# Kernel optimization log

Hardware: AMD Instinct MI355X
Metric: run time of the kernel (lower is better)

Reference implementation:

```python
import jax, jax.numpy as jnp
import numpy as np

NEG_INF = -10000000000.0
HEADS = 16


def setup_inputs() -> dict:
    key = jax.random.key(0)
    ks = jax.random.split(key, 12)
    B, S, E = 2, 2048, 1024
    sc = 1.0 / np.sqrt(E)
    inp = {
        "input_queries": jax.random.normal(ks[0], (B, S, E), jnp.float32),
        "input_keys": jax.random.normal(ks[1], (B, S, E), jnp.float32),
        "input_values": jax.random.normal(ks[2], (B, S, E), jnp.float32),
        # causal mask: True where attention is disallowed (masked_fill where mask==True)
        "mask": jnp.triu(jnp.ones((S, S), jnp.bool_), k=1)[None, None],
        "Wq": jax.random.normal(ks[3], (E, E), jnp.float32) * sc,
        "bq": jax.random.normal(ks[4], (E,), jnp.float32) * 0.01,
        "Wk": jax.random.normal(ks[5], (E, E), jnp.float32) * sc,
        "bk": jax.random.normal(ks[6], (E,), jnp.float32) * 0.01,
        "Wv": jax.random.normal(ks[7], (E, E), jnp.float32) * sc,
        "bv": jax.random.normal(ks[8], (E,), jnp.float32) * 0.01,
        "Wo": jax.random.normal(ks[9], (E, E), jnp.float32) * sc,
        "bo": jax.random.normal(ks[10], (E,), jnp.float32) * 0.01,
    }
    return inp


def reference(input_queries, input_keys, input_values, mask, Wq, bq, Wk, bk, Wv, bv, Wo, bo):
    B, S, E = input_queries.shape
    H = HEADS
    D = E // H
    # torch Linear: y = x @ W.T + b
    q = (input_queries @ Wq.T + bq).reshape(B, S, H, D).transpose(0, 2, 1, 3)  # bhsd
    k = (input_keys @ Wk.T + bk).reshape(B, S, H, D).transpose(0, 2, 1, 3)
    v = (input_values @ Wv.T + bv).reshape(B, S, H, D).transpose(0, 2, 1, 3)
    scores = jnp.einsum('bhqd,bhkd->bhqk', q, k) / jnp.sqrt(jnp.asarray(D, q.dtype))
    scores = jnp.where(mask, jnp.asarray(NEG_INF, scores.dtype), scores)
    attn = jax.nn.softmax(scores, axis=-1)
    out = jnp.einsum('bhqk,bhkd->bhqd', attn, v).transpose(0, 2, 1, 3).reshape(B, S, E)
    return out @ Wo.T + bo
```

## Files before the change

kernel.cpp:

```cpp
#include <hip/hip_runtime.h>
#include <hip/hip_bf16.h>

#define DEVI __device__ __forceinline__

using bf16x8 = __attribute__((ext_vector_type(8))) short;
using f32x4  = __attribute__((ext_vector_type(4))) float;
using f32x16 = __attribute__((ext_vector_type(16))) float;

#define LOG2E 1.4426950408889634f

DEVI unsigned short f2bf(float f){
  unsigned int u = __float_as_uint(f);
  return (unsigned short)((u + 0x7fffu + ((u>>16)&1u)) >> 16);
}

DEVI unsigned int cvt_pk_bf16(float lo, float hi){
  unsigned int r;
  asm("v_cvt_pk_bf16_f32 %0, %1, %2" : "=v"(r) : "v"(lo), "v"(hi));
  return r;
}

#if __has_builtin(__builtin_amdgcn_exp2f)
#define EXP2(x) __builtin_amdgcn_exp2f(x)
#else
#define EXP2(x) exp2f(x)
#endif

DEVI void gload_lds16(const unsigned short* src, unsigned short* lds){
  __builtin_amdgcn_global_load_lds((const __attribute__((address_space(1))) void*)src,
                                   (__attribute__((address_space(3))) void*)lds, 16, 0, 0);
}

DEVI bf16x8 mk8(unsigned w0, unsigned w1, unsigned w2, unsigned w3){
  union { unsigned u[4]; bf16x8 v; } x;
  x.u[0]=w0; x.u[1]=w1; x.u[2]=w2; x.u[3]=w3;
  return x.v;
}

__global__ __launch_bounds__(256) void convert_kernel(
  const float* __restrict__ Xq, const float* __restrict__ Xk, const float* __restrict__ Xv,
  const float* __restrict__ Wq, const float* __restrict__ Wk, const float* __restrict__ Wv,
  const float* __restrict__ Wo, unsigned short* __restrict__ ws)
{
  const int y = blockIdx.y;
  const float* src;
  unsigned short* dst;
  int n4;
  if (y < 3){
    src = (y==0)?Xq:((y==1)?Xk:Xv);
    dst = ws + (size_t)y*4194304;
    n4 = 1048576;
  } else {
    src = (y==3)?Wq:((y==4)?Wk:((y==5)?Wv:Wo));
    dst = ws + 12582912 + (size_t)(y-3)*1048576;
    n4 = 262144;
  }
  const int stride = gridDim.x * 256;
  for (int i = blockIdx.x*256 + threadIdx.x; i < n4; i += stride){
    float4 v = ((const float4*)src)[i];
    uint2 u;
    u.x = cvt_pk_bf16(v.x, v.y);
    u.y = cvt_pk_bf16(v.z, v.w);
    ((uint2*)dst)[i] = u;
  }
}

__global__ __launch_bounds__(256) void proj_qkv_kernel(
  const unsigned short* __restrict__ Xb, const unsigned short* __restrict__ Wb,
  const float* __restrict__ Bq, const float* __restrict__ Bk, const float* __restrict__ Bv,
  unsigned short* __restrict__ Qo, unsigned short* __restrict__ Ko, unsigned short* __restrict__ Vo)
{
  const int p = blockIdx.y;
  const unsigned short* __restrict__ A = Xb + (size_t)p*4194304;
  const unsigned short* __restrict__ B = Wb + (size_t)p*1048576;
  const float* __restrict__ Bb = (p==0)?Bq:((p==1)?Bk:Bv);
  unsigned short* __restrict__ Out = (p==0)?Qo:((p==1)?Ko:Vo);
  const float oscale = (p==0)?(0.125f*LOG2E):1.0f;

  const int tm = blockIdx.x >> 3, tn = blockIdx.x & 7;
  const int m0 = tm*128, n0 = tn*128;
  const int tid = threadIdx.x;
  const int w = tid>>6, l = tid&63;
  const int wr = w>>1, wc = w&1;
  const int lg = l>>4, lr = l&15;

  __shared__ unsigned short As[128*64];
  __shared__ unsigned short Bs[128*64];

  f32x4 acc[4][4];
  #pragma unroll
  for (int i=0;i<4;i++)
    #pragma unroll
    for (int j=0;j<4;j++){ f32x4 z = {0.f,0.f,0.f,0.f}; acc[i][j] = z; }

  for (int kt=0; kt<1024; kt+=64){
    #pragma unroll
    for (int i=0;i<4;i++){
      int rbase = w*32 + i*8;
      gload_lds16(A + (size_t)(m0 + rbase + (l>>3))*1024 + kt + (l&7)*8, As + rbase*64);
      gload_lds16(B + (size_t)(n0 + rbase + (l>>3))*1024 + kt + (l&7)*8, Bs + rbase*64);
    }
    __syncthreads();

    #pragma unroll
    for (int ck=0;ck<2;ck++){
      bf16x8 af[4], bfr[4];
      #pragma unroll
      for (int f=0;f<4;f++){
        af[f]  = *(const bf16x8*)(As + (wr*64 + f*16 + lr)*64 + ck*32 + lg*8);
        bfr[f] = *(const bf16x8*)(Bs + (wc*64 + f*16 + lr)*64 + ck*32 + lg*8);
      }
      #pragma unroll
      for (int fr=0;fr<4;fr++)
        #pragma unroll
        for (int fc=0;fc<4;fc++)
          acc[fr][fc] = __builtin_amdgcn_mfma_f32_16x16x32_bf16(af[fr], bfr[fc], acc[fr][fc], 0,0,0);
    }
    __syncthreads();
  }

  if (p == 2){
    #pragma unroll
    for (int fc=0;fc<4;fc++){
      int n = n0 + wc*64 + fc*16 + lr;
      float bias = Bb[n];
      int h = n>>6, d = n&63;
      #pragma unroll
      for (int fr=0;fr<4;fr++){
        int m = m0 + wr*64 + fr*16 + lg*4;
        int b = m>>11, s = m & 2047;
        uint2 u;
        u.x = cvt_pk_bf16(acc[fr][fc][0]+bias, acc[fr][fc][1]+bias);
        u.y = cvt_pk_bf16(acc[fr][fc][2]+bias, acc[fr][fc][3]+bias);
        *(uint2*)(Out + (((size_t)((b<<4)+h)*64 + d)*2048 + s)) = u;
      }
    }
  } else {
    #pragma unroll
    for (int fc=0;fc<4;fc++){
      int n = n0 + wc*64 + fc*16 + lr;
      float bias = Bb[n];
      int h = n>>6, d = n&63;
      #pragma unroll
      for (int fr=0;fr<4;fr++){
        #pragma unroll
        for (int r=0;r<4;r++){
          int m = m0 + wr*64 + fr*16 + lg*4 + r;
          int b = m>>11, s = m & 2047;
          float v = (acc[fr][fc][r] + bias) * oscale;
          Out[ ((size_t)((b<<4)+h)*2048 + (size_t)s)*64 + d ] = f2bf(v);
        }
      }
    }
  }
}

__global__ __launch_bounds__(256,2) void attn_kernel(
  const unsigned short* __restrict__ Q, const unsigned short* __restrict__ Kg,
  const unsigned short* __restrict__ Vt, unsigned short* __restrict__ AO)
{
  const int idx = blockIdx.x;
  const int qt = 15 - (idx >> 5);
  const int bh = idx & 31;
  const size_t base = (size_t)bh * 131072;
  const int q0 = qt * 128;
  const int tid = threadIdx.x, w = tid>>6, l = tid&63;
  const int lq = l & 31, hi = l >> 5;
  const int qq = q0 + w*32 + lq;

  __shared__ unsigned short Ks[2][4096];
  __shared__ unsigned short Vs[2][4096];

  bf16x8 qf[4];
  {
    const unsigned short* qp = Q + base + (size_t)qq*64;
    #pragma unroll
    for (int s=0;s<4;s++) qf[s] = *(const bf16x8*)(qp + s*16 + hi*8);
  }

  f32x16 oacc[2];
  #pragma unroll
  for (int dt=0;dt<2;dt++)
    #pragma unroll
    for (int r=0;r<16;r++) oacc[dt][r] = 0.f;
  float m_i = -INFINITY, l_i = 0.f;

  const int NT = 2*qt + 2;

  auto stage = [&](int kt, int half){
    const int kv0 = kt*64;
    #pragma unroll
    for (int i=0;i<2;i++){
      int c = tid + i*256;
      int row = c>>3;
      int kc = (c&7) ^ (row&7);
      gload_lds16(Kg + base + (size_t)(kv0+row)*64 + kc*8, &Ks[half][0] + c*8);
      gload_lds16(Vt + base + (size_t)row*2048 + kv0 + kc*8, &Vs[half][0] + c*8);
    }
  };

  stage(0, 0);
  __syncthreads();

  for (int kt=0; kt<NT; kt++){
    const int cur = kt & 1;
    if (kt+1 < NT) stage(kt+1, cur^1);
    const int kv0 = kt*64;

    f32x16 sacc[2];
    #pragma unroll
    for (int kvt=0;kvt<2;kvt++)
      #pragma unroll
      for (int r=0;r<16;r++) sacc[kvt][r] = 0.f;

    __builtin_amdgcn_s_setprio(1);
    #pragma unroll
    for (int kvt=0;kvt<2;kvt++){
      int row = kvt*32 + lq;
      const char* kb = (const char*)&Ks[cur][0] + row*128;
      int swz = (row&7)<<4;
      #pragma unroll
      for (int s=0;s<4;s++){
        bf16x8 kf = *(const bf16x8*)(kb + ((s*32 + hi*16) ^ swz));
        sacc[kvt] = __builtin_amdgcn_mfma_f32_32x32x16_bf16(kf, qf[s], sacc[kvt], 0,0,0);
      }
    }
    __builtin_amdgcn_s_setprio(0);

    #pragma unroll
    for (int kvt=0;kvt<2;kvt++){
      if (kv0 + kvt*32 + 31 > q0 + w*32){
        #pragma unroll
        for (int r=0;r<16;r++){
          int kvv = kv0 + kvt*32 + (r&3) + 8*(r>>2) + 4*hi;
          if (kvv > qq) sacc[kvt][r] = -1e30f;
        }
      }
    }

    float mt = sacc[0][0];
    #pragma unroll
    for (int kvt=0;kvt<2;kvt++)
      #pragma unroll
      for (int r=0;r<16;r++) mt = fmaxf(mt, sacc[kvt][r]);
    mt = fmaxf(mt, __shfl_xor(mt, 32));

    if (__any(mt > m_i + 8.f)){
      float mn = fmaxf(m_i, mt);
      float sc = EXP2(m_i - mn);
      m_i = mn;
      l_i *= sc;
      #pragma unroll
      for (int dt=0;dt<2;dt++)
        #pragma unroll
        for (int r=0;r<16;r++) oacc[dt][r] *= sc;
    }
    float rs = 0.f;
    #pragma unroll
    for (int kvt=0;kvt<2;kvt++)
      #pragma unroll
      for (int r=0;r<16;r++){
        float pv = EXP2(sacc[kvt][r] - m_i);
        sacc[kvt][r] = pv;
        rs += pv;
      }
    rs += __shfl_xor(rs, 32);
    l_i += rs;

    unsigned pa[8], pb[8], sa[8], sb[8];
    #pragma unroll
    for (int g=0; g<8; g++){
      int kvt = g>>2, gl = g&3;
      pa[g] = cvt_pk_bf16(sacc[kvt][4*gl+0], sacc[kvt][4*gl+1]);
      pb[g] = cvt_pk_bf16(sacc[kvt][4*gl+2], sacc[kvt][4*gl+3]);
      sa[g] = __shfl_xor(pa[g], 32);
      sb[g] = __shfl_xor(pb[g], 32);
    }
    bf16x8 pfrag[4];
    #pragma unroll
    for (int s=0;s<4;s++){
      int g0 = (s>>1)*4 + 2*(s&1);
      unsigned w0 = hi ? sa[g0+1] : pa[g0];
      unsigned w1 = hi ? sb[g0+1] : pb[g0];
      unsigned w2 = hi ? pa[g0+1] : sa[g0];
      unsigned w3 = hi ? pb[g0+1] : sb[g0];
      pfrag[s] = mk8(w0, w1, w2, w3);
    }

    __builtin_amdgcn_s_setprio(1);
    #pragma unroll
    for (int dt=0;dt<2;dt++){
      int row = dt*32 + lq;
      const char* vb = (const char*)&Vs[cur][0] + row*128;
      int swz = (row&7)<<4;
      #pragma unroll
      for (int s=0;s<4;s++){
        bf16x8 vf = *(const bf16x8*)(vb + ((s*32 + hi*16) ^ swz));
        oacc[dt] = __builtin_amdgcn_mfma_f32_32x32x16_bf16(vf, pfrag[s], oacc[dt], 0,0,0);
      }
    }
    __builtin_amdgcn_s_setprio(0);

    __syncthreads();
  }

  unsigned short* Es = &Ks[0][0] + w*2048;
  float inv = 1.0f / l_i;
  {
    char* eb = (char*)Es + lq*128;
    int swz = (lq&7)<<4;
    #pragma unroll
    for (int dt=0;dt<2;dt++)
      #pragma unroll
      for (int g=0;g<4;g++){
        int d0 = dt*32 + 8*g + 4*hi;
        unsigned u0 = cvt_pk_bf16(oacc[dt][4*g+0]*inv, oacc[dt][4*g+1]*inv);
        unsigned u1 = cvt_pk_bf16(oacc[dt][4*g+2]*inv, oacc[dt][4*g+3]*inv);
        *(unsigned*)(eb + ((d0*2    ) ^ swz)) = u0;
        *(unsigned*)(eb + ((d0*2 + 4) ^ swz)) = u1;
      }
  }
  const int b = bh>>4, h = bh&15;
  {
    const char* rb = (const char*)Es + lq*128;
    int swz = (lq&7)<<4;
    unsigned short* op = AO + ((size_t)b*2048 + (q0 + w*32 + lq))*1024 + h*64 + hi*32;
    #pragma unroll
    for (int j=0;j<2;j++){
      bf16x8 v = *(const bf16x8*)(rb + ((hi*64 + j*16) ^ swz));
      *(bf16x8*)(op + j*8) = v;
    }
    #pragma unroll
    for (int j=2;j<4;j++){
      bf16x8 v = *(const bf16x8*)(rb + ((hi*64 + j*16) ^ swz));
      *(bf16x8*)(op + j*8) = v;
    }
  }
}

__global__ __launch_bounds__(256) void proj_out_kernel(
  const unsigned short* __restrict__ A, const unsigned short* __restrict__ B,
  const float* __restrict__ Bb, float* __restrict__ Out)
{
  const int tm = blockIdx.x >> 3, tn = blockIdx.x & 7;
  const int m0 = tm*128, n0 = tn*128;
  const int tid = threadIdx.x;
  const int w = tid>>6, l = tid&63;
  const int wr = w>>1, wc = w&1;
  const int lg = l>>4, lr = l&15;

  __shared__ unsigned short As[128*64];
  __shared__ unsigned short Bs[128*64];

  f32x4 acc[4][4];
  #pragma unroll
  for (int i=0;i<4;i++)
    #pragma unroll
    for (int j=0;j<4;j++){ f32x4 z = {0.f,0.f,0.f,0.f}; acc[i][j] = z; }

  for (int kt=0; kt<1024; kt+=64){
    #pragma unroll
    for (int i=0;i<4;i++){
      int rbase = w*32 + i*8;
      gload_lds16(A + (size_t)(m0 + rbase + (l>>3))*1024 + kt + (l&7)*8, As + rbase*64);
      gload_lds16(B + (size_t)(n0 + rbase + (l>>3))*1024 + kt + (l&7)*8, Bs + rbase*64);
    }
    __syncthreads();

    #pragma unroll
    for (int ck=0;ck<2;ck++){
      bf16x8 af[4], bfr[4];
      #pragma unroll
      for (int f=0;f<4;f++){
        af[f]  = *(const bf16x8*)(As + (wr*64 + f*16 + lr)*64 + ck*32 + lg*8);
        bfr[f] = *(const bf16x8*)(Bs + (wc*64 + f*16 + lr)*64 + ck*32 + lg*8);
      }
      #pragma unroll
      for (int fr=0;fr<4;fr++)
        #pragma unroll
        for (int fc=0;fc<4;fc++)
          acc[fr][fc] = __builtin_amdgcn_mfma_f32_16x16x32_bf16(af[fr], bfr[fc], acc[fr][fc], 0,0,0);
    }
    __syncthreads();
  }

  #pragma unroll
  for (int fc=0;fc<4;fc++){
    int n = n0 + wc*64 + fc*16 + lr;
    float bias = Bb[n];
    #pragma unroll
    for (int fr=0;fr<4;fr++){
      #pragma unroll
      for (int r=0;r<4;r++){
        int m = m0 + wr*64 + fr*16 + lg*4 + r;
        Out[(size_t)m*1024 + n] = acc[fr][fc][r] + bias;
      }
    }
  }
}

extern "C" void kernel_launch(void* const* d_in, const int* in_sizes, int n_in,
                              void* d_out, int out_size, void* d_ws, size_t ws_size,
                              hipStream_t stream)
{
  const float* Xq = (const float*)d_in[0];
  const float* Xk = (const float*)d_in[1];
  const float* Xv = (const float*)d_in[2];
  const float* Wq = (const float*)d_in[4];
  const float* bq = (const float*)d_in[5];
  const float* Wk = (const float*)d_in[6];
  const float* bk = (const float*)d_in[7];
  const float* Wv = (const float*)d_in[8];
  const float* bv = (const float*)d_in[9];
  const float* Wo = (const float*)d_in[10];
  const float* bo = (const float*)d_in[11];

  unsigned short* ws  = (unsigned short*)d_ws;
  unsigned short* Xb  = ws;
  unsigned short* Wb  = ws + 12582912;
  unsigned short* Qw  = ws + 16777216;
  unsigned short* Kw  = ws + 20971520;
  unsigned short* Vw  = ws + 25165824;
  unsigned short* AOw = ws + 29360128;
  float* out = (float*)d_out;

  convert_kernel<<<dim3(512,7), 256, 0, stream>>>(Xq,Xk,Xv,Wq,Wk,Wv,Wo, ws);
  proj_qkv_kernel<<<dim3(256,3), 256, 0, stream>>>(Xb, Wb, bq,bk,bv, Qw,Kw,Vw);
  attn_kernel<<<512, 256, 0, stream>>>(Qw,Kw,Vw,AOw);
  proj_out_kernel<<<256, 256, 0, stream>>>(AOw, Wb + 3*1048576, bo, out);
}
```

Before: 254.7 us.

## Double-buffer GEMM LDS tiles, XOR-swizzle LDS layout, remap blocks per XCD

Both projection GEMMs now double-buffer the A/B tiles in LDS, so the global-to-LDS load of the next K-slice overlaps the MFMA work on the current one. LDS rows are XOR-swizzled by row index to avoid bank conflicts on the fragment reads. Block indices are remapped so each XCD gets contiguous M-tiles that share A rows, which should improve L2 reuse. The price is twice the LDS per block, which may lower occupancy.

Measured after the change: 249.2 us. -2.2%, faster.

```diff
diff --git a/kernel.cpp b/kernel.cpp
--- a/kernel.cpp
+++ b/kernel.cpp
@@ -70,22 +70,27 @@
   const float* __restrict__ Bq, const float* __restrict__ Bk, const float* __restrict__ Bv,
   unsigned short* __restrict__ Qo, unsigned short* __restrict__ Ko, unsigned short* __restrict__ Vo)
 {
-  const int p = blockIdx.y;
+  const int L = blockIdx.x;
+  const int xcd = L & 7, g = L >> 3;
+  const int combo = xcd*12 + (g>>3);
+  const int tn = g & 7;
+  const int p  = combo >> 5;
+  const int tm = combo & 31;
+
   const unsigned short* __restrict__ A = Xb + (size_t)p*4194304;
   const unsigned short* __restrict__ B = Wb + (size_t)p*1048576;
   const float* __restrict__ Bb = (p==0)?Bq:((p==1)?Bk:Bv);
   unsigned short* __restrict__ Out = (p==0)?Qo:((p==1)?Ko:Vo);
   const float oscale = (p==0)?(0.125f*LOG2E):1.0f;
 
-  const int tm = blockIdx.x >> 3, tn = blockIdx.x & 7;
   const int m0 = tm*128, n0 = tn*128;
   const int tid = threadIdx.x;
   const int w = tid>>6, l = tid&63;
   const int wr = w>>1, wc = w&1;
   const int lg = l>>4, lr = l&15;
 
-  __shared__ unsigned short As[128*64];
-  __shared__ unsigned short Bs[128*64];
+  __shared__ unsigned short As[2][8192];
+  __shared__ unsigned short Bs[2][8192];
 
   f32x4 acc[4][4];
   #pragma unroll
@@ -93,22 +98,34 @@
     #pragma unroll
     for (int j=0;j<4;j++){ f32x4 z = {0.f,0.f,0.f,0.f}; acc[i][j] = z; }
 
-  for (int kt=0; kt<1024; kt+=64){
+  const int sub = l>>3;
+  const int kc  = (l&7) ^ sub;
+  auto stage = [&](int kt, int h){
     #pragma unroll
     for (int i=0;i<4;i++){
       int rbase = w*32 + i*8;
-      gload_lds16(A + (size_t)(m0 + rbase + (l>>3))*1024 + kt + (l&7)*8, As + rbase*64);
-      gload_lds16(B + (size_t)(n0 + rbase + (l>>3))*1024 + kt + (l&7)*8, Bs + rbase*64);
-    }
-    __syncthreads();
+      gload_lds16(A + (size_t)(m0+rbase+sub)*1024 + kt + kc*8, &As[h][0] + rbase*64);
+      gload_lds16(B + (size_t)(n0+rbase+sub)*1024 + kt + kc*8, &Bs[h][0] + rbase*64);
+    }
+  };
+
+  stage(0, 0);
+  asm volatile("s_waitcnt vmcnt(0)" ::: "memory");
+  __builtin_amdgcn_s_barrier();
+
+  int cur = 0;
+  for (int kt6=0; kt6<16; kt6++){
+    if (kt6 < 15) stage((kt6+1)*64, cur^1);
 
     #pragma unroll
     for (int ck=0;ck<2;ck++){
       bf16x8 af[4], bfr[4];
       #pragma unroll
       for (int f=0;f<4;f++){
-        af[f]  = *(const bf16x8*)(As + (wr*64 + f*16 + lr)*64 + ck*32 + lg*8);
-        bfr[f] = *(const bf16x8*)(Bs + (wc*64 + f*16 + lr)*64 + ck*32 + lg*8);
+        int ra = wr*64 + f*16 + lr;
+        af[f]  = *(const bf16x8*)((const char*)&As[cur][0] + ra*128 + ((ck*64 + lg*16) ^ ((ra&7)<<4)));
+        int rb = wc*64 + f*16 + lr;
+        bfr[f] = *(const bf16x8*)((const char*)&Bs[cur][0] + rb*128 + ((ck*64 + lg*16) ^ ((rb&7)<<4)));
       }
       #pragma unroll
       for (int fr=0;fr<4;fr++)
@@ -116,7 +133,10 @@
         for (int fc=0;fc<4;fc++)
           acc[fr][fc] = __builtin_amdgcn_mfma_f32_16x16x32_bf16(af[fr], bfr[fc], acc[fr][fc], 0,0,0);
     }
-    __syncthreads();
+
+    asm volatile("s_waitcnt vmcnt(0)" ::: "memory");
+    __builtin_amdgcn_s_barrier();
+    cur ^= 1;
   }
 
   if (p == 2){
@@ -342,15 +362,18 @@
   const unsigned short* __restrict__ A, const unsigned short* __restrict__ B,
   const float* __restrict__ Bb, float* __restrict__ Out)
 {
-  const int tm = blockIdx.x >> 3, tn = blockIdx.x & 7;
+  const int L = blockIdx.x;
+  const int xcd = L & 7, g = L >> 3;
+  const int tm = xcd*4 + (g>>3);
+  const int tn = g & 7;
   const int m0 = tm*128, n0 = tn*128;
   const int tid = threadIdx.x;
   const int w = tid>>6, l = tid&63;
   const int wr = w>>1, wc = w&1;
   const int lg = l>>4, lr = l&15;
 
-  __shared__ unsigned short As[128*64];
-  __shared__ unsigned short Bs[128*64];
+  __shared__ unsigned short As[2][8192];
+  __shared__ unsigned short Bs[2][8192];
 
   f32x4 acc[4][4];
   #pragma unroll
@@ -358,22 +381,34 @@
     #pragma unroll
     for (int j=0;j<4;j++){ f32x4 z = {0.f,0.f,0.f,0.f}; acc[i][j] = z; }
 
-  for (int kt=0; kt<1024; kt+=64){
+  const int sub = l>>3;
+  const int kc  = (l&7) ^ sub;
+  auto stage = [&](int kt, int h){
     #pragma unroll
     for (int i=0;i<4;i++){
       int rbase = w*32 + i*8;
-      gload_lds16(A + (size_t)(m0 + rbase + (l>>3))*1024 + kt + (l&7)*8, As + rbase*64);
-      gload_lds16(B + (size_t)(n0 + rbase + (l>>3))*1024 + kt + (l&7)*8, Bs + rbase*64);
-    }
-    __syncthreads();
+      gload_lds16(A + (size_t)(m0+rbase+sub)*1024 + kt + kc*8, &As[h][0] + rbase*64);
+      gload_lds16(B + (size_t)(n0+rbase+sub)*1024 + kt + kc*8, &Bs[h][0] + rbase*64);
+    }
+  };
+
+  stage(0, 0);
+  asm volatile("s_waitcnt vmcnt(0)" ::: "memory");
+  __builtin_amdgcn_s_barrier();
+
+  int cur = 0;
+  for (int kt6=0; kt6<16; kt6++){
+    if (kt6 < 15) stage((kt6+1)*64, cur^1);
 
     #pragma unroll
     for (int ck=0;ck<2;ck++){
       bf16x8 af[4], bfr[4];
       #pragma unroll
       for (int f=0;f<4;f++){
-        af[f]  = *(const bf16x8*)(As + (wr*64 + f*16 + lr)*64 + ck*32 + lg*8);
-        bfr[f] = *(const bf16x8*)(Bs + (wc*64 + f*16 + lr)*64 + ck*32 + lg*8);
+        int ra = wr*64 + f*16 + lr;
+        af[f]  = *(const bf16x8*)((const char*)&As[cur][0] + ra*128 + ((ck*64 + lg*16) ^ ((ra&7)<<4)));
+        int rb = wc*64 + f*16 + lr;
+        bfr[f] = *(const bf16x8*)((const char*)&Bs[cur][0] + rb*128 + ((ck*64 + lg*16) ^ ((rb&7)<<4)));
       }
       #pragma unroll
       for (int fr=0;fr<4;fr++)
@@ -381,7 +416,10 @@
         for (int fc=0;fc<4;fc++)
           acc[fr][fc] = __builtin_amdgcn_mfma_f32_16x16x32_bf16(af[fr], bfr[fc], acc[fr][fc], 0,0,0);
     }
-    __syncthreads();
+
+    asm volatile("s_waitcnt vmcnt(0)" ::: "memory");
+    __builtin_amdgcn_s_barrier();
+    cur ^= 1;
   }
 
   #pragma unroll
@@ -425,7 +463,7 @@
   float* out = (float*)d_out;
 
   convert_kernel<<<dim3(512,7), 256, 0, stream>>>(Xq,Xk,Xv,Wq,Wk,Wv,Wo, ws);
-  proj_qkv_kernel<<<dim3(256,3), 256, 0, stream>>>(Xb, Wb, bq,bk,bv, Qw,Kw,Vw);
+  proj_qkv_kernel<<<768, 256, 0, stream>>>(Xb, Wb, bq,bk,bv, Qw,Kw,Vw);
   attn_kernel<<<512, 256, 0, stream>>>(Qw,Kw,Vw,AOw);
   proj_out_kernel<<<256, 256, 0, stream>>>(AOw, Wb + 3*1048576, bo, out);
 }
```
